# Kernel tuning notes

Hardware: AMD Instinct MI355X
Metric: run time of the kernel (lower is better)

Reference implementation:

```python
import jax, jax.numpy as jnp
import numpy as np

E = 32      # particle_embed_dim = q/k/v head out dim
G = 2       # nof_net_types (conv groups)
NEG_SLOPE = 0.01


def _glin(x, w, b, groups):
    """Grouped 1x1 conv on (M, C, 1, 1) == grouped linear.
    x: (M, Cin), w: (Cout, Cin//groups), b: (Cout,)."""
    M = x.shape[0]
    Cout = w.shape[0]
    xg = x.reshape(M, groups, -1)                 # (M, G, Cin/G)
    wg = w.reshape(groups, Cout // groups, -1)    # (G, Cout/G, Cin/G)
    y = jnp.einsum('mgi,goi->mgo', xg, wg).reshape(M, Cout)
    return y + b


def setup_inputs() -> dict:
    key = jax.random.key(0)
    ks = jax.random.split(key, 9)
    B, N = 32, 1024
    s = 0.05
    return {
        'x_e':   jax.random.normal(ks[0], (B, N, G * E), dtype=jnp.float32),
        'w_qkv': jax.random.normal(ks[1], (3 * G * E, E), dtype=jnp.float32) * s,
        'b_qkv': jax.random.normal(ks[2], (3 * G * E,), dtype=jnp.float32) * s,
        'w_h1':  jax.random.normal(ks[3], (G * E, 2 * E), dtype=jnp.float32) * s,
        'b_h1':  jax.random.normal(ks[4], (G * E,), dtype=jnp.float32) * s,
        'w_h10': jax.random.normal(ks[5], (G * E, E), dtype=jnp.float32) * s,
        'b_h10': jax.random.normal(ks[6], (G * E,), dtype=jnp.float32) * s,
        'w_h11': jax.random.normal(ks[7], (G * E, E), dtype=jnp.float32) * s,
        'b_h11': jax.random.normal(ks[8], (G * E,), dtype=jnp.float32) * s,
    }


def reference(x_e, w_qkv, b_qkv, w_h1, b_h1, w_h10, b_h10, w_h11, b_h11):
    B, N, D = x_e.shape                      # D = G*E = 64
    act = lambda z: jnp.where(z >= 0, z, NEG_SLOPE * z)

    # grouped 1x1-conv QKV projection
    qkv = _glin(x_e.reshape(B * N, D), w_qkv, b_qkv, G)        # (B*N, 3*G*E)
    qkv = qkv.reshape(B, N, G, 3, E).transpose(0, 2, 3, 1, 4)  # (B, G, 3, N, E)
    q, k, v = qkv[:, :, 0], qkv[:, :, 1], qkv[:, :, 2]         # each (B, G, N, E)

    # NOTE: module divides k by sqrt(E) and logits by sqrt(E) again -> 1/E total
    scale = 1.0 / E
    ip = jnp.einsum('bgne,bgme->bgnm', q, k) * scale           # (B, G, N, N)
    sip = jax.nn.softmax(ip, axis=-1)
    attn = jnp.einsum('bgnm,bgme->bgne', sip, v)               # (B, G, N, E)

    # concat pre-attention v with attention output, regroup per-particle
    x_xe = jnp.concatenate([v, attn], axis=3)                  # (B, G, N, 2E)
    x_xe = x_xe.transpose(0, 2, 1, 3).reshape(B * N, G * 2 * E)  # (B*N, 128)

    h = act(_glin(x_xe, w_h1, b_h1, G))
    h = act(_glin(h, w_h10, b_h10, G))
    h = act(_glin(h, w_h11, b_h11, G))
    return h.reshape(B * N, G * E, 1, 1)
```

## Files before the change

### kernel.cpp

```cpp
#include <hip/hip_runtime.h>

#define B_ 32
#define N_ 1024
#define G_ 2
#define E_ 32
#define M_ (B_*N_)
#define NEG 0.01f
#define QT 128
#define KT 128
#define QSC (1.4426950408889634f/32.0f)

using half8  = __attribute__((ext_vector_type(8))) _Float16;
using half4  = __attribute__((ext_vector_type(4))) _Float16;
using floatx4 = __attribute__((ext_vector_type(4))) float;

#if defined(__has_builtin)
#if __has_builtin(__builtin_amdgcn_exp2f)
#define EXP2(x) __builtin_amdgcn_exp2f(x)
#endif
#endif
#ifndef EXP2
#define EXP2(x) exp2f(x)
#endif

__global__ __launch_bounds__(256) void qkv_kernel(
    const float* __restrict__ x, const float* __restrict__ w, const float* __restrict__ bias,
    _Float16* __restrict__ Qh, _Float16* __restrict__ Kh,
    _Float16* __restrict__ Vh, _Float16* __restrict__ Vth)
{
    __shared__ _Float16 wsh[192*36];
    __shared__ float bsh[192];
    int t = threadIdx.x;
    for (int idx = t; idx < 192*32; idx += 256) {
        int r = idx >> 5, c = idx & 31;
        wsh[r*36 + c] = (_Float16)w[idx];
    }
    if (t < 192) bsh[t] = bias[t];
    __syncthreads();

    int lane = t & 63, wv = t >> 6;
    int L15 = lane & 15, quad = lane >> 4;
    int row0 = blockIdx.x*64 + wv*16;
    int b = row0 >> 10, nn0 = row0 & 1023;

    half4 ax[2][2];
    #pragma unroll
    for (int g2 = 0; g2 < 2; g2++)
        #pragma unroll
        for (int kt = 0; kt < 2; kt++) {
            float4 f = *(const float4*)(x + (size_t)(row0+L15)*64 + g2*32 + kt*16 + quad*4);
            half4 h = { (_Float16)f.x, (_Float16)f.y, (_Float16)f.z, (_Float16)f.w };
            ax[g2][kt] = h;
        }

    floatx4 acc[12];
    #pragma unroll
    for (int i = 0; i < 12; i++) acc[i] = (floatx4){0.f,0.f,0.f,0.f};

    #pragma unroll
    for (int g2 = 0; g2 < 2; g2++)
        #pragma unroll
        for (int nt = 0; nt < 6; nt++)
            #pragma unroll
            for (int kt = 0; kt < 2; kt++) {
                half4 bw = *(const half4*)&wsh[(g2*96+nt*16+L15)*36 + kt*16 + quad*4];
                acc[g2*6+nt] = __builtin_amdgcn_mfma_f32_16x16x16f16(ax[g2][kt], bw, acc[g2*6+nt], 0,0,0);
            }

    #pragma unroll
    for (int g2 = 0; g2 < 2; g2++) {
        size_t bg = (size_t)(b*2 + g2);
        #pragma unroll
        for (int nt = 0; nt < 6; nt++) {
            float bia = bsh[g2*96 + nt*16 + L15];
            floatx4 a4 = acc[g2*6+nt];
            int e = (nt & 1)*16 + L15;
            int kind = nt >> 1;
            if (kind == 0) {
                #pragma unroll
                for (int r = 0; r < 4; r++) {
                    int nn = nn0 + quad*4 + r;
                    Qh[(bg*N_ + nn)*32 + e] = (_Float16)((a4[r] + bia)*QSC);
                }
            } else if (kind == 1) {
                #pragma unroll
                for (int r = 0; r < 4; r++) {
                    int nn = nn0 + quad*4 + r;
                    Kh[(bg*N_ + nn)*32 + e] = (_Float16)(a4[r] + bia);
                }
            } else {
                half4 vv;
                #pragma unroll
                for (int r = 0; r < 4; r++) {
                    int nn = nn0 + quad*4 + r;
                    float vval = a4[r] + bia;
                    Vh[(bg*N_ + nn)*32 + e] = (_Float16)vval;
                    vv[r] = (_Float16)vval;
                }
                *(half4*)(Vth + (bg*32 + e)*N_ + nn0 + quad*4) = vv;
            }
        }
    }
}

struct __align__(16) SmemU {
    union {
        struct { _Float16 Kst[128*40]; _Float16 Vtst[32*136]; } a;
        _Float16 xs[128*72];
    } u;
    float linv[128];
    float bl1[32], bl10[32], bl11[32];
};

__global__ __launch_bounds__(256) void attn_mlp_kernel(
    const _Float16* __restrict__ Qh, const _Float16* __restrict__ Kh,
    const _Float16* __restrict__ Vh, const _Float16* __restrict__ Vth,
    const float* __restrict__ w_h1,  const float* __restrict__ b_h1,
    const float* __restrict__ w_h10, const float* __restrict__ b_h10,
    const float* __restrict__ w_h11, const float* __restrict__ b_h11,
    float* __restrict__ out)
{
    __shared__ SmemU sm;
    int t = threadIdx.x;
    int bg = blockIdx.x >> 3;
    int qtile = blockIdx.x & 7;
    int b = bg >> 1, g = bg & 1;
    int qbase = qtile * QT;
    size_t bgN = (size_t)bg * N_;

    if (t < 32) {
        sm.bl1[t]  = b_h1[g*32+t];
        sm.bl10[t] = b_h10[g*32+t];
        sm.bl11[t] = b_h11[g*32+t];
    }

    int lane = t & 63;
    int w    = t >> 6;
    int L15  = lane & 15;
    int quad = lane >> 4;
    int q0w  = qbase + w*32;

    half8 bq0 = *(const half8*)(Qh + (bgN + q0w +      L15)*32 + quad*8);
    half8 bq1 = *(const half8*)(Qh + (bgN + q0w + 16 + L15)*32 + quad*8);

    floatx4 o00 = {0.f,0.f,0.f,0.f}, o01 = o00, o10 = o00, o11 = o00;
    float lsum0 = 0.f, lsum1 = 0.f;

    for (int kt = 0; kt < N_/KT; kt++) {
        __syncthreads();
        #pragma unroll
        for (int it = 0; it < 2; it++) {
            int idx = t + it*256;
            int row = idx >> 2, c = idx & 3;
            half8 kv = *(const half8*)(Kh + (bgN + (size_t)kt*KT + row)*32 + c*8);
            *(half8*)&sm.u.a.Kst[row*40 + c*8] = kv;
        }
        #pragma unroll
        for (int it = 0; it < 2; it++) {
            int idx = t + it*256;
            int ee = idx >> 4, c = idx & 15;
            half8 vv = *(const half8*)(Vth + (size_t)bg*(32*N_) + (size_t)ee*N_ + kt*KT + c*8);
            *(half8*)&sm.u.a.Vtst[ee*136 + c*8] = vv;
        }
        __syncthreads();

        #pragma unroll
        for (int mt = 0; mt < 8; mt++) {
            half8 ak = *(const half8*)&sm.u.a.Kst[(mt*16 + L15)*40 + quad*8];
            floatx4 z = {0.f,0.f,0.f,0.f};
            floatx4 s0 = __builtin_amdgcn_mfma_f32_16x16x32_f16(ak, bq0, z, 0, 0, 0);
            floatx4 s1 = __builtin_amdgcn_mfma_f32_16x16x32_f16(ak, bq1, z, 0, 0, 0);
            float p00 = EXP2(s0.x), p01 = EXP2(s0.y), p02 = EXP2(s0.z), p03 = EXP2(s0.w);
            float p10 = EXP2(s1.x), p11 = EXP2(s1.y), p12 = EXP2(s1.z), p13 = EXP2(s1.w);
            lsum0 += (p00+p01)+(p02+p03);
            lsum1 += (p10+p11)+(p12+p13);
            half4 a0 = { (_Float16)p00, (_Float16)p01, (_Float16)p02, (_Float16)p03 };
            half4 a1 = { (_Float16)p10, (_Float16)p11, (_Float16)p12, (_Float16)p13 };
            half4 bv0 = *(const half4*)&sm.u.a.Vtst[      L15*136 + mt*16 + quad*4];
            half4 bv1 = *(const half4*)&sm.u.a.Vtst[(16+L15)*136 + mt*16 + quad*4];
            o00 = __builtin_amdgcn_mfma_f32_16x16x16f16(a0, bv0, o00, 0, 0, 0);
            o01 = __builtin_amdgcn_mfma_f32_16x16x16f16(a0, bv1, o01, 0, 0, 0);
            o10 = __builtin_amdgcn_mfma_f32_16x16x16f16(a1, bv0, o10, 0, 0, 0);
            o11 = __builtin_amdgcn_mfma_f32_16x16x16f16(a1, bv1, o11, 0, 0, 0);
        }
    }

    lsum0 += __shfl_xor(lsum0, 16, 64); lsum0 += __shfl_xor(lsum0, 32, 64);
    lsum1 += __shfl_xor(lsum1, 16, 64); lsum1 += __shfl_xor(lsum1, 32, 64);
    if (quad == 0) {
        sm.linv[w*32 +      L15] = 1.0f / lsum0;
        sm.linv[w*32 + 16 + L15] = 1.0f / lsum1;
    }
    __syncthreads();

    for (int idx = t; idx < 512; idx += 256) {
        int row = idx >> 2, c = idx & 3;
        half8 vv = *(const half8*)(Vh + (bgN + qbase + row)*32 + c*8);
        *(half8*)&sm.u.xs[row*72 + c*8] = vv;
    }
    {
        const floatx4* ofr[2][2] = { {&o00,&o01}, {&o10,&o11} };
        #pragma unroll
        for (int nt = 0; nt < 2; nt++) {
            float4 li = *(const float4*)&sm.linv[w*32 + nt*16 + quad*4];
            #pragma unroll
            for (int et = 0; et < 2; et++) {
                floatx4 ov = *ofr[nt][et];
                sm.u.xs[(w*32+nt*16+quad*4+0)*72 + 32 + et*16 + L15] = (_Float16)(ov[0]*li.x);
                sm.u.xs[(w*32+nt*16+quad*4+1)*72 + 32 + et*16 + L15] = (_Float16)(ov[1]*li.y);
                sm.u.xs[(w*32+nt*16+quad*4+2)*72 + 32 + et*16 + L15] = (_Float16)(ov[2]*li.z);
                sm.u.xs[(w*32+nt*16+quad*4+3)*72 + 32 + et*16 + L15] = (_Float16)(ov[3]*li.w);
            }
        }
    }
    __syncthreads();

    half4 a1f[2][4], a2f[2][2], a3f[2][2];
    #pragma unroll
    for (int mt = 0; mt < 2; mt++) {
        #pragma unroll
        for (int kt = 0; kt < 4; kt++) {
            float4 f = *(const float4*)(w_h1 + (size_t)(g*32+mt*16+L15)*64 + kt*16 + quad*4);
            half4 h = { (_Float16)f.x, (_Float16)f.y, (_Float16)f.z, (_Float16)f.w };
            a1f[mt][kt] = h;
        }
        #pragma unroll
        for (int kt = 0; kt < 2; kt++) {
            float4 f = *(const float4*)(w_h10 + (size_t)(g*32+mt*16+L15)*32 + kt*16 + quad*4);
            half4 h = { (_Float16)f.x, (_Float16)f.y, (_Float16)f.z, (_Float16)f.w };
            a2f[mt][kt] = h;
            float4 f2 = *(const float4*)(w_h11 + (size_t)(g*32+mt*16+L15)*32 + kt*16 + quad*4);
            half4 h2 = { (_Float16)f2.x, (_Float16)f2.y, (_Float16)f2.z, (_Float16)f2.w };
            a3f[mt][kt] = h2;
        }
    }

    floatx4 d1[2][2];
    #pragma unroll
    for (int mt = 0; mt < 2; mt++)
        #pragma unroll
        for (int nt = 0; nt < 2; nt++) d1[mt][nt] = (floatx4){0.f,0.f,0.f,0.f};
    #pragma unroll
    for (int nt = 0; nt < 2; nt++)
        #pragma unroll
        for (int kt = 0; kt < 4; kt++) {
            half4 b1 = *(const half4*)&sm.u.xs[(w*32+nt*16+L15)*72 + kt*16 + quad*4];
            d1[0][nt] = __builtin_amdgcn_mfma_f32_16x16x16f16(a1f[0][kt], b1, d1[0][nt], 0,0,0);
            d1[1][nt] = __builtin_amdgcn_mfma_f32_16x16x16f16(a1f[1][kt], b1, d1[1][nt], 0,0,0);
        }
    half4 h1b[2][2];
    #pragma unroll
    for (int mt = 0; mt < 2; mt++) {
        float4 bb = *(const float4*)&sm.bl1[mt*16 + quad*4];
        #pragma unroll
        for (int nt = 0; nt < 2; nt++) {
            float v0 = d1[mt][nt][0] + bb.x; v0 = (v0>=0.f)?v0:NEG*v0;
            float v1 = d1[mt][nt][1] + bb.y; v1 = (v1>=0.f)?v1:NEG*v1;
            float v2 = d1[mt][nt][2] + bb.z; v2 = (v2>=0.f)?v2:NEG*v2;
            float v3 = d1[mt][nt][3] + bb.w; v3 = (v3>=0.f)?v3:NEG*v3;
            half4 h = { (_Float16)v0, (_Float16)v1, (_Float16)v2, (_Float16)v3 };
            h1b[mt][nt] = h;
        }
    }
    floatx4 d2[2][2];
    #pragma unroll
    for (int mt = 0; mt < 2; mt++)
        #pragma unroll
        for (int nt = 0; nt < 2; nt++) d2[mt][nt] = (floatx4){0.f,0.f,0.f,0.f};
    #pragma unroll
    for (int mt = 0; mt < 2; mt++)
        #pragma unroll
        for (int nt = 0; nt < 2; nt++)
            #pragma unroll
            for (int kt = 0; kt < 2; kt++)
                d2[mt][nt] = __builtin_amdgcn_mfma_f32_16x16x16f16(a2f[mt][kt], h1b[kt][nt], d2[mt][nt], 0,0,0);
    half4 h2b[2][2];
    #pragma unroll
    for (int mt = 0; mt < 2; mt++) {
        float4 bb = *(const float4*)&sm.bl10[mt*16 + quad*4];
        #pragma unroll
        for (int nt = 0; nt < 2; nt++) {
            float v0 = d2[mt][nt][0] + bb.x; v0 = (v0>=0.f)?v0:NEG*v0;
            float v1 = d2[mt][nt][1] + bb.y; v1 = (v1>=0.f)?v1:NEG*v1;
            float v2 = d2[mt][nt][2] + bb.z; v2 = (v2>=0.f)?v2:NEG*v2;
            float v3 = d2[mt][nt][3] + bb.w; v3 = (v3>=0.f)?v3:NEG*v3;
            half4 h = { (_Float16)v0, (_Float16)v1, (_Float16)v2, (_Float16)v3 };
            h2b[mt][nt] = h;
        }
    }
    floatx4 d3[2][2];
    #pragma unroll
    for (int mt = 0; mt < 2; mt++)
        #pragma unroll
        for (int nt = 0; nt < 2; nt++) d3[mt][nt] = (floatx4){0.f,0.f,0.f,0.f};
    #pragma unroll
    for (int mt = 0; mt < 2; mt++)
        #pragma unroll
        for (int nt = 0; nt < 2; nt++)
            #pragma unroll
            for (int kt = 0; kt < 2; kt++)
                d3[mt][nt] = __builtin_amdgcn_mfma_f32_16x16x16f16(a3f[mt][kt], h2b[kt][nt], d3[mt][nt], 0,0,0);
    #pragma unroll
    for (int mt = 0; mt < 2; mt++) {
        float4 bb = *(const float4*)&sm.bl11[mt*16 + quad*4];
        #pragma unroll
        for (int nt = 0; nt < 2; nt++) {
            size_t rowbase = ((size_t)b*N_ + qbase + w*32 + nt*16 + L15)*64 + g*32 + mt*16 + quad*4;
            float v0 = d3[mt][nt][0] + bb.x; out[rowbase+0] = (v0>=0.f)?v0:NEG*v0;
            float v1 = d3[mt][nt][1] + bb.y; out[rowbase+1] = (v1>=0.f)?v1:NEG*v1;
            float v2 = d3[mt][nt][2] + bb.z; out[rowbase+2] = (v2>=0.f)?v2:NEG*v2;
            float v3 = d3[mt][nt][3] + bb.w; out[rowbase+3] = (v3>=0.f)?v3:NEG*v3;
        }
    }
}

extern "C" void kernel_launch(void* const* d_in, const int* in_sizes, int n_in,
                              void* d_out, int out_size, void* d_ws, size_t ws_size,
                              hipStream_t stream) {
    const float* x_e   = (const float*)d_in[0];
    const float* w_qkv = (const float*)d_in[1];
    const float* b_qkv = (const float*)d_in[2];
    const float* w_h1  = (const float*)d_in[3];
    const float* b_h1  = (const float*)d_in[4];
    const float* w_h10 = (const float*)d_in[5];
    const float* b_h10 = (const float*)d_in[6];
    const float* w_h11 = (const float*)d_in[7];
    const float* b_h11 = (const float*)d_in[8];
    float* out = (float*)d_out;

    const size_t qkv_elems = (size_t)B_*G_*N_*E_;
    _Float16* Qh  = (_Float16*)d_ws;
    _Float16* Kh  = Qh + qkv_elems;
    _Float16* Vh  = Kh + qkv_elems;
    _Float16* Vth = Vh + qkv_elems;

    hipLaunchKernelGGL(qkv_kernel, dim3(M_/64), dim3(256), 0, stream,
                       x_e, w_qkv, b_qkv, Qh, Kh, Vh, Vth);
    hipLaunchKernelGGL(attn_mlp_kernel, dim3(B_*G_*(N_/QT)), dim3(256), 0, stream,
                       Qh, Kh, Vh, Vth, w_h1, b_h1, w_h10, b_h10, w_h11, b_h11, out);
}
```

Measured before the change: 105.7 us.

## Double-buffer K/V tiles, stage QKV stores through LDS, pack conversions

The attention loop now double-buffers the K and V-transpose tiles in shared memory, loading the next tile into registers while the current one is computed, which removes one barrier per iteration. The QKV kernel stages Q/K/V/Vt in LDS and writes them with coalesced 16-byte stores instead of scattered 2-byte stores. Packed fp32->fp16 round-toward-zero conversions replace scalar casts, MLP biases seed the accumulators, and output stores become float4. Shared memory use grows, and launch_bounds now requests two blocks per CU, which may limit registers; rtz rounding slightly changes numerics.

```diff
diff --git a/kernel.cpp b/kernel.cpp
--- a/kernel.cpp
+++ b/kernel.cpp
@@ -2,16 +2,13 @@
 
 #define B_ 32
 #define N_ 1024
-#define G_ 2
-#define E_ 32
-#define M_ (B_*N_)
 #define NEG 0.01f
-#define QT 128
-#define KT 128
 #define QSC (1.4426950408889634f/32.0f)
 
 using half8  = __attribute__((ext_vector_type(8))) _Float16;
 using half4  = __attribute__((ext_vector_type(4))) _Float16;
+using half2  = __attribute__((ext_vector_type(2))) _Float16;
+using fp16x2 = __attribute__((ext_vector_type(2))) __fp16;
 using floatx4 = __attribute__((ext_vector_type(4))) float;
 
 #if defined(__has_builtin)
@@ -23,6 +20,11 @@
 #define EXP2(x) exp2f(x)
 #endif
 
+__device__ inline half2 pkcvt(float a, float b) {
+    fp16x2 r = __builtin_amdgcn_cvt_pkrtz(a, b);
+    return __builtin_bit_cast(half2, r);
+}
+
 __global__ __launch_bounds__(256) void qkv_kernel(
     const float* __restrict__ x, const float* __restrict__ w, const float* __restrict__ bias,
     _Float16* __restrict__ Qh, _Float16* __restrict__ Kh,
@@ -30,6 +32,8 @@
 {
     __shared__ _Float16 wsh[192*36];
     __shared__ float bsh[192];
+    __shared__ _Float16 sQ[64*72], sK[64*72], sV[64*72];
+    __shared__ _Float16 vT[64*72];
     int t = threadIdx.x;
     for (int idx = t; idx < 192*32; idx += 256) {
         int r = idx >> 5, c = idx & 31;
@@ -41,7 +45,7 @@
     int lane = t & 63, wv = t >> 6;
     int L15 = lane & 15, quad = lane >> 4;
     int row0 = blockIdx.x*64 + wv*16;
-    int b = row0 >> 10, nn0 = row0 & 1023;
+    int b = row0 >> 10, nn0g = (blockIdx.x*64) & 1023;
 
     half4 ax[2][2];
     #pragma unroll
@@ -49,7 +53,9 @@
         #pragma unroll
         for (int kt = 0; kt < 2; kt++) {
             float4 f = *(const float4*)(x + (size_t)(row0+L15)*64 + g2*32 + kt*16 + quad*4);
-            half4 h = { (_Float16)f.x, (_Float16)f.y, (_Float16)f.z, (_Float16)f.w };
+            half2 ha = pkcvt(f.x, f.y);
+            half2 hb = pkcvt(f.z, f.w);
+            half4 h = { ha[0], ha[1], hb[0], hb[1] };
             ax[g2][kt] = h;
         }
 
@@ -69,50 +75,60 @@
 
     #pragma unroll
     for (int g2 = 0; g2 < 2; g2++) {
-        size_t bg = (size_t)(b*2 + g2);
         #pragma unroll
         for (int nt = 0; nt < 6; nt++) {
             float bia = bsh[g2*96 + nt*16 + L15];
             floatx4 a4 = acc[g2*6+nt];
             int e = (nt & 1)*16 + L15;
             int kind = nt >> 1;
+            int rbase = wv*16 + quad*4;
             if (kind == 0) {
                 #pragma unroll
-                for (int r = 0; r < 4; r++) {
-                    int nn = nn0 + quad*4 + r;
-                    Qh[(bg*N_ + nn)*32 + e] = (_Float16)((a4[r] + bia)*QSC);
-                }
+                for (int r = 0; r < 4; r++)
+                    sQ[(rbase+r)*72 + g2*32 + e] = (_Float16)((a4[r] + bia)*QSC);
             } else if (kind == 1) {
                 #pragma unroll
-                for (int r = 0; r < 4; r++) {
-                    int nn = nn0 + quad*4 + r;
-                    Kh[(bg*N_ + nn)*32 + e] = (_Float16)(a4[r] + bia);
-                }
+                for (int r = 0; r < 4; r++)
+                    sK[(rbase+r)*72 + g2*32 + e] = (_Float16)(a4[r] + bia);
             } else {
                 half4 vv;
                 #pragma unroll
                 for (int r = 0; r < 4; r++) {
-                    int nn = nn0 + quad*4 + r;
                     float vval = a4[r] + bia;
-                    Vh[(bg*N_ + nn)*32 + e] = (_Float16)vval;
+                    sV[(rbase+r)*72 + g2*32 + e] = (_Float16)vval;
                     vv[r] = (_Float16)vval;
                 }
-                *(half4*)(Vth + (bg*32 + e)*N_ + nn0 + quad*4) = vv;
+                *(half4*)&vT[(g2*32+e)*72 + rbase] = vv;
             }
         }
     }
+    __syncthreads();
+
+    int r = t >> 2, c8 = t & 3;
+    #pragma unroll
+    for (int g2 = 0; g2 < 2; g2++) {
+        size_t gbase = (((size_t)(b*2+g2))*N_ + nn0g + r)*32 + c8*8;
+        *(half8*)(Qh + gbase) = *(const half8*)&sQ[r*72 + g2*32 + c8*8];
+        *(half8*)(Kh + gbase) = *(const half8*)&sK[r*72 + g2*32 + c8*8];
+        *(half8*)(Vh + gbase) = *(const half8*)&sV[r*72 + g2*32 + c8*8];
+    }
+    #pragma unroll
+    for (int it = 0; it < 2; it++) {
+        int idx = t + it*256;
+        int ge = idx >> 3, c = idx & 7;
+        *(half8*)(Vth + ((size_t)(b*2)*32 + ge)*N_ + nn0g + c*8) = *(const half8*)&vT[ge*72 + c*8];
+    }
 }
 
-struct __align__(16) SmemU {
-    union {
-        struct { _Float16 Kst[128*40]; _Float16 Vtst[32*136]; } a;
-        _Float16 xs[128*72];
-    } u;
+struct __align__(16) SmemB {
+    _Float16 Kst[2][128*40];
+    _Float16 Vtst[2][32*136];
+    _Float16 xs[128*72];
     float linv[128];
     float bl1[32], bl10[32], bl11[32];
 };
 
-__global__ __launch_bounds__(256) void attn_mlp_kernel(
+__global__ __launch_bounds__(256, 2) void attn_mlp_kernel(
     const _Float16* __restrict__ Qh, const _Float16* __restrict__ Kh,
     const _Float16* __restrict__ Vh, const _Float16* __restrict__ Vth,
     const float* __restrict__ w_h1,  const float* __restrict__ b_h1,
@@ -120,13 +136,15 @@
     const float* __restrict__ w_h11, const float* __restrict__ b_h11,
     float* __restrict__ out)
 {
-    __shared__ SmemU sm;
+    __shared__ SmemB sm;
     int t = threadIdx.x;
     int bg = blockIdx.x >> 3;
     int qtile = blockIdx.x & 7;
     int b = bg >> 1, g = bg & 1;
-    int qbase = qtile * QT;
+    int qbase = qtile * 128;
     size_t bgN = (size_t)bg * N_;
+    int lane = t & 63, w = t >> 6;
+    int L15 = lane & 15, quad = lane >> 4;
 
     if (t < 32) {
         sm.bl1[t]  = b_h1[g*32+t];
@@ -134,55 +152,65 @@
         sm.bl11[t] = b_h11[g*32+t];
     }
 
-    int lane = t & 63;
-    int w    = t >> 6;
-    int L15  = lane & 15;
-    int quad = lane >> 4;
-    int q0w  = qbase + w*32;
-
-    half8 bq0 = *(const half8*)(Qh + (bgN + q0w +      L15)*32 + quad*8);
-    half8 bq1 = *(const half8*)(Qh + (bgN + q0w + 16 + L15)*32 + quad*8);
-
-    floatx4 o00 = {0.f,0.f,0.f,0.f}, o01 = o00, o10 = o00, o11 = o00;
-    float lsum0 = 0.f, lsum1 = 0.f;
-
-    for (int kt = 0; kt < N_/KT; kt++) {
-        __syncthreads();
+    half8 bq0 = *(const half8*)(Qh + (bgN + qbase + w*32 +      L15)*32 + quad*8);
+    half8 bq1 = *(const half8*)(Qh + (bgN + qbase + w*32 + 16 + L15)*32 + quad*8);
+
+    float4 kr[2], vr[2];
+    auto ld = [&](int kt) {
         #pragma unroll
         for (int it = 0; it < 2; it++) {
             int idx = t + it*256;
             int row = idx >> 2, c = idx & 3;
-            half8 kv = *(const half8*)(Kh + (bgN + (size_t)kt*KT + row)*32 + c*8);
-            *(half8*)&sm.u.a.Kst[row*40 + c*8] = kv;
-        }
+            kr[it] = *(const float4*)(Kh + (bgN + (size_t)kt*128 + row)*32 + c*8);
+            int e = idx >> 4, cc = idx & 15;
+            vr[it] = *(const float4*)(Vth + ((size_t)bg*32 + e)*N_ + (size_t)kt*128 + cc*8);
+        }
+    };
+    auto st = [&](int buf) {
         #pragma unroll
         for (int it = 0; it < 2; it++) {
             int idx = t + it*256;
-            int ee = idx >> 4, c = idx & 15;
-            half8 vv = *(const half8*)(Vth + (size_t)bg*(32*N_) + (size_t)ee*N_ + kt*KT + c*8);
-            *(half8*)&sm.u.a.Vtst[ee*136 + c*8] = vv;
-        }
-        __syncthreads();
-
-        #pragma unroll
-        for (int mt = 0; mt < 8; mt++) {
-            half8 ak = *(const half8*)&sm.u.a.Kst[(mt*16 + L15)*40 + quad*8];
-            floatx4 z = {0.f,0.f,0.f,0.f};
-            floatx4 s0 = __builtin_amdgcn_mfma_f32_16x16x32_f16(ak, bq0, z, 0, 0, 0);
-            floatx4 s1 = __builtin_amdgcn_mfma_f32_16x16x32_f16(ak, bq1, z, 0, 0, 0);
+            int row = idx >> 2, c = idx & 3;
+            *(float4*)&sm.Kst[buf][row*40 + c*8] = kr[it];
+            int e = idx >> 4, cc = idx & 15;
+            *(float4*)&sm.Vtst[buf][e*136 + cc*8] = vr[it];
+        }
+    };
+
+    ld(0); st(0);
+    __syncthreads();
+
+    floatx4 o00 = {0.f,0.f,0.f,0.f}, o01 = o00, o10 = o00, o11 = o00;
+    float lsum0 = 0.f, lsum1 = 0.f;
+
+    for (int kt = 0; kt < 8; kt++) {
+        int cur = kt & 1;
+        if (kt < 7) ld(kt + 1);
+        #pragma unroll
+        for (int m8 = 0; m8 < 8; m8++) {
+            half8 ak = *(const half8*)&sm.Kst[cur][(m8*16 + L15)*40 + quad*8];
+            floatx4 zz = {0.f,0.f,0.f,0.f};
+            floatx4 s0 = __builtin_amdgcn_mfma_f32_16x16x32_f16(ak, bq0, zz, 0,0,0);
+            floatx4 s1 = __builtin_amdgcn_mfma_f32_16x16x32_f16(ak, bq1, zz, 0,0,0);
             float p00 = EXP2(s0.x), p01 = EXP2(s0.y), p02 = EXP2(s0.z), p03 = EXP2(s0.w);
             float p10 = EXP2(s1.x), p11 = EXP2(s1.y), p12 = EXP2(s1.z), p13 = EXP2(s1.w);
             lsum0 += (p00+p01)+(p02+p03);
             lsum1 += (p10+p11)+(p12+p13);
-            half4 a0 = { (_Float16)p00, (_Float16)p01, (_Float16)p02, (_Float16)p03 };
-            half4 a1 = { (_Float16)p10, (_Float16)p11, (_Float16)p12, (_Float16)p13 };
-            half4 bv0 = *(const half4*)&sm.u.a.Vtst[      L15*136 + mt*16 + quad*4];
-            half4 bv1 = *(const half4*)&sm.u.a.Vtst[(16+L15)*136 + mt*16 + quad*4];
-            o00 = __builtin_amdgcn_mfma_f32_16x16x16f16(a0, bv0, o00, 0, 0, 0);
-            o01 = __builtin_amdgcn_mfma_f32_16x16x16f16(a0, bv1, o01, 0, 0, 0);
-            o10 = __builtin_amdgcn_mfma_f32_16x16x16f16(a1, bv0, o10, 0, 0, 0);
-            o11 = __builtin_amdgcn_mfma_f32_16x16x16f16(a1, bv1, o11, 0, 0, 0);
-        }
+            half2 pa = pkcvt(p00, p01);
+            half2 pb = pkcvt(p02, p03);
+            half2 pc = pkcvt(p10, p11);
+            half2 pd = pkcvt(p12, p13);
+            half4 a0 = { pa[0], pa[1], pb[0], pb[1] };
+            half4 a1 = { pc[0], pc[1], pd[0], pd[1] };
+            half4 bv0 = *(const half4*)&sm.Vtst[cur][      L15*136 + m8*16 + quad*4];
+            half4 bv1 = *(const half4*)&sm.Vtst[cur][(16 + L15)*136 + m8*16 + quad*4];
+            o00 = __builtin_amdgcn_mfma_f32_16x16x16f16(a0, bv0, o00, 0,0,0);
+            o01 = __builtin_amdgcn_mfma_f32_16x16x16f16(a0, bv1, o01, 0,0,0);
+            o10 = __builtin_amdgcn_mfma_f32_16x16x16f16(a1, bv0, o10, 0,0,0);
+            o11 = __builtin_amdgcn_mfma_f32_16x16x16f16(a1, bv1, o11, 0,0,0);
+        }
+        if (kt < 7) st(1 - cur);
+        __syncthreads();
     }
 
     lsum0 += __shfl_xor(lsum0, 16, 64); lsum0 += __shfl_xor(lsum0, 32, 64);
@@ -191,12 +219,12 @@
         sm.linv[w*32 +      L15] = 1.0f / lsum0;
         sm.linv[w*32 + 16 + L15] = 1.0f / lsum1;
     }
-    __syncthreads();
-
-    for (int idx = t; idx < 512; idx += 256) {
+
+    #pragma unroll
+    for (int it = 0; it < 2; it++) {
+        int idx = t + it*256;
         int row = idx >> 2, c = idx & 3;
-        half8 vv = *(const half8*)(Vh + (bgN + qbase + row)*32 + c*8);
-        *(half8*)&sm.u.xs[row*72 + c*8] = vv;
+        *(half8*)&sm.xs[row*72 + c*8] = *(const half8*)(Vh + (bgN + qbase + row)*32 + c*8);
     }
     {
         const floatx4* ofr[2][2] = { {&o00,&o01}, {&o10,&o11} };
@@ -206,10 +234,10 @@
             #pragma unroll
             for (int et = 0; et < 2; et++) {
                 floatx4 ov = *ofr[nt][et];
-                sm.u.xs[(w*32+nt*16+quad*4+0)*72 + 32 + et*16 + L15] = (_Float16)(ov[0]*li.x);
-                sm.u.xs[(w*32+nt*16+quad*4+1)*72 + 32 + et*16 + L15] = (_Float16)(ov[1]*li.y);
-                sm.u.xs[(w*32+nt*16+quad*4+2)*72 + 32 + et*16 + L15] = (_Float16)(ov[2]*li.z);
-                sm.u.xs[(w*32+nt*16+quad*4+3)*72 + 32 + et*16 + L15] = (_Float16)(ov[3]*li.w);
+                sm.xs[(w*32+nt*16+quad*4+0)*72 + 32 + et*16 + L15] = (_Float16)(ov[0]*li.x);
+                sm.xs[(w*32+nt*16+quad*4+1)*72 + 32 + et*16 + L15] = (_Float16)(ov[1]*li.y);
+                sm.xs[(w*32+nt*16+quad*4+2)*72 + 32 + et*16 + L15] = (_Float16)(ov[2]*li.z);
+                sm.xs[(w*32+nt*16+quad*4+3)*72 + 32 + et*16 + L15] = (_Float16)(ov[3]*li.w);
             }
         }
     }
@@ -221,52 +249,62 @@
         #pragma unroll
         for (int kt = 0; kt < 4; kt++) {
             float4 f = *(const float4*)(w_h1 + (size_t)(g*32+mt*16+L15)*64 + kt*16 + quad*4);
-            half4 h = { (_Float16)f.x, (_Float16)f.y, (_Float16)f.z, (_Float16)f.w };
+            half2 ha = pkcvt(f.x, f.y);
+            half2 hb = pkcvt(f.z, f.w);
+            half4 h = { ha[0], ha[1], hb[0], hb[1] };
             a1f[mt][kt] = h;
         }
         #pragma unroll
         for (int kt = 0; kt < 2; kt++) {
             float4 f = *(const float4*)(w_h10 + (size_t)(g*32+mt*16+L15)*32 + kt*16 + quad*4);
-            half4 h = { (_Float16)f.x, (_Float16)f.y, (_Float16)f.z, (_Float16)f.w };
+            half2 ha = pkcvt(f.x, f.y);
+            half2 hb = pkcvt(f.z, f.w);
+            half4 h = { ha[0], ha[1], hb[0], hb[1] };
             a2f[mt][kt] = h;
             float4 f2 = *(const float4*)(w_h11 + (size_t)(g*32+mt*16+L15)*32 + kt*16 + quad*4);
-            half4 h2 = { (_Float16)f2.x, (_Float16)f2.y, (_Float16)f2.z, (_Float16)f2.w };
+            half2 hc = pkcvt(f2.x, f2.y);
+            half2 hd = pkcvt(f2.z, f2.w);
+            half4 h2 = { hc[0], hc[1], hd[0], hd[1] };
             a3f[mt][kt] = h2;
         }
     }
 
     floatx4 d1[2][2];
     #pragma unroll
-    for (int mt = 0; mt < 2; mt++)
-        #pragma unroll
-        for (int nt = 0; nt < 2; nt++) d1[mt][nt] = (floatx4){0.f,0.f,0.f,0.f};
+    for (int mt = 0; mt < 2; mt++) {
+        float4 bb = *(const float4*)&sm.bl1[mt*16 + quad*4];
+        floatx4 seed = { bb.x, bb.y, bb.z, bb.w };
+        d1[mt][0] = seed; d1[mt][1] = seed;
+    }
     #pragma unroll
     for (int nt = 0; nt < 2; nt++)
         #pragma unroll
         for (int kt = 0; kt < 4; kt++) {
-            half4 b1 = *(const half4*)&sm.u.xs[(w*32+nt*16+L15)*72 + kt*16 + quad*4];
+            half4 b1 = *(const half4*)&sm.xs[(w*32+nt*16+L15)*72 + kt*16 + quad*4];
             d1[0][nt] = __builtin_amdgcn_mfma_f32_16x16x16f16(a1f[0][kt], b1, d1[0][nt], 0,0,0);
             d1[1][nt] = __builtin_amdgcn_mfma_f32_16x16x16f16(a1f[1][kt], b1, d1[1][nt], 0,0,0);
         }
     half4 h1b[2][2];
     #pragma unroll
+    for (int mt = 0; mt < 2; mt++)
+        #pragma unroll
+        for (int nt = 0; nt < 2; nt++) {
+            float v0 = d1[mt][nt][0]; v0 = (v0>=0.f)?v0:NEG*v0;
+            float v1 = d1[mt][nt][1]; v1 = (v1>=0.f)?v1:NEG*v1;
+            float v2 = d1[mt][nt][2]; v2 = (v2>=0.f)?v2:NEG*v2;
+            float v3 = d1[mt][nt][3]; v3 = (v3>=0.f)?v3:NEG*v3;
+            half2 ha = pkcvt(v0, v1);
+            half2 hb = pkcvt(v2, v3);
+            half4 h = { ha[0], ha[1], hb[0], hb[1] };
+            h1b[mt][nt] = h;
+        }
+    floatx4 d2[2][2];
+    #pragma unroll
     for (int mt = 0; mt < 2; mt++) {
-        float4 bb = *(const float4*)&sm.bl1[mt*16 + quad*4];
-        #pragma unroll
-        for (int nt = 0; nt < 2; nt++) {
-            float v0 = d1[mt][nt][0] + bb.x; v0 = (v0>=0.f)?v0:NEG*v0;
-            float v1 = d1[mt][nt][1] + bb.y; v1 = (v1>=0.f)?v1:NEG*v1;
-            float v2 = d1[mt][nt][2] + bb.z; v2 = (v2>=0.f)?v2:NEG*v2;
-            float v3 = d1[mt][nt][3] + bb.w; v3 = (v3>=0.f)?v3:NEG*v3;
-            half4 h = { (_Float16)v0, (_Float16)v1, (_Float16)v2, (_Float16)v3 };
-            h1b[mt][nt] = h;
-        }
-    }
-    floatx4 d2[2][2];
-    #pragma unroll
-    for (int mt = 0; mt < 2; mt++)
-        #pragma unroll
-        for (int nt = 0; nt < 2; nt++) d2[mt][nt] = (floatx4){0.f,0.f,0.f,0.f};
+        float4 bb = *(const float4*)&sm.bl10[mt*16 + quad*4];
+        floatx4 seed = { bb.x, bb.y, bb.z, bb.w };
+        d2[mt][0] = seed; d2[mt][1] = seed;
+    }
     #pragma unroll
     for (int mt = 0; mt < 2; mt++)
         #pragma unroll
@@ -276,23 +314,25 @@
                 d2[mt][nt] = __builtin_amdgcn_mfma_f32_16x16x16f16(a2f[mt][kt], h1b[kt][nt], d2[mt][nt], 0,0,0);
     half4 h2b[2][2];
     #pragma unroll
+    for (int mt = 0; mt < 2; mt++)
+        #pragma unroll
+        for (int nt = 0; nt < 2; nt++) {
+            float v0 = d2[mt][nt][0]; v0 = (v0>=0.f)?v0:NEG*v0;
+            float v1 = d2[mt][nt][1]; v1 = (v1>=0.f)?v1:NEG*v1;
+            float v2 = d2[mt][nt][2]; v2 = (v2>=0.f)?v2:NEG*v2;
+            float v3 = d2[mt][nt][3]; v3 = (v3>=0.f)?v3:NEG*v3;
+            half2 ha = pkcvt(v0, v1);
+            half2 hb = pkcvt(v2, v3);
+            half4 h = { ha[0], ha[1], hb[0], hb[1] };
+            h2b[mt][nt] = h;
+        }
+    floatx4 d3[2][2];
+    #pragma unroll
     for (int mt = 0; mt < 2; mt++) {
-        float4 bb = *(const float4*)&sm.bl10[mt*16 + quad*4];
-        #pragma unroll
-        for (int nt = 0; nt < 2; nt++) {
-            float v0 = d2[mt][nt][0] + bb.x; v0 = (v0>=0.f)?v0:NEG*v0;
-            float v1 = d2[mt][nt][1] + bb.y; v1 = (v1>=0.f)?v1:NEG*v1;
-            float v2 = d2[mt][nt][2] + bb.z; v2 = (v2>=0.f)?v2:NEG*v2;
-            float v3 = d2[mt][nt][3] + bb.w; v3 = (v3>=0.f)?v3:NEG*v3;
-            half4 h = { (_Float16)v0, (_Float16)v1, (_Float16)v2, (_Float16)v3 };
-            h2b[mt][nt] = h;
-        }
-    }
-    floatx4 d3[2][2];
-    #pragma unroll
-    for (int mt = 0; mt < 2; mt++)
-        #pragma unroll
-        for (int nt = 0; nt < 2; nt++) d3[mt][nt] = (floatx4){0.f,0.f,0.f,0.f};
+        float4 bb = *(const float4*)&sm.bl11[mt*16 + quad*4];
+        floatx4 seed = { bb.x, bb.y, bb.z, bb.w };
+        d3[mt][0] = seed; d3[mt][1] = seed;
+    }
     #pragma unroll
     for (int mt = 0; mt < 2; mt++)
         #pragma unroll
@@ -301,17 +341,16 @@
             for (int kt = 0; kt < 2; kt++)
                 d3[mt][nt] = __builtin_amdgcn_mfma_f32_16x16x16f16(a3f[mt][kt], h2b[kt][nt], d3[mt][nt], 0,0,0);
     #pragma unroll
-    for (int mt = 0; mt < 2; mt++) {
-        float4 bb = *(const float4*)&sm.bl11[mt*16 + quad*4];
+    for (int mt = 0; mt < 2; mt++)
         #pragma unroll
         for (int nt = 0; nt < 2; nt++) {
-            size_t rowbase = ((size_t)b*N_ + qbase + w*32 + nt*16 + L15)*64 + g*32 + mt*16 + quad*4;
-            float v0 = d3[mt][nt][0] + bb.x; out[rowbase+0] = (v0>=0.f)?v0:NEG*v0;
-            float v1 = d3[mt][nt][1] + bb.y; out[rowbase+1] = (v1>=0.f)?v1:NEG*v1;
-            float v2 = d3[mt][nt][2] + bb.z; out[rowbase+2] = (v2>=0.f)?v2:NEG*v2;
-            float v3 = d3[mt][nt][3] + bb.w; out[rowbase+3] = (v3>=0.f)?v3:NEG*v3;
-        }
-    }
+            float4 ov;
+            ov.x = d3[mt][nt][0]; ov.x = (ov.x>=0.f)?ov.x:NEG*ov.x;
+            ov.y = d3[mt][nt][1]; ov.y = (ov.y>=0.f)?ov.y:NEG*ov.y;
+            ov.z = d3[mt][nt][2]; ov.z = (ov.z>=0.f)?ov.z:NEG*ov.z;
+            ov.w = d3[mt][nt][3]; ov.w = (ov.w>=0.f)?ov.w:NEG*ov.w;
+            *(float4*)(out + ((size_t)b*N_ + qbase + w*32 + nt*16 + L15)*64 + g*32 + mt*16 + quad*4) = ov;
+        }
 }
 
 extern "C" void kernel_launch(void* const* d_in, const int* in_sizes, int n_in,
@@ -328,14 +367,14 @@
     const float* b_h11 = (const float*)d_in[8];
     float* out = (float*)d_out;
 
-    const size_t qkv_elems = (size_t)B_*G_*N_*E_;
+    const size_t qkv_elems = (size_t)B_*2*N_*32;
     _Float16* Qh  = (_Float16*)d_ws;
     _Float16* Kh  = Qh + qkv_elems;
     _Float16* Vh  = Kh + qkv_elems;
     _Float16* Vth = Vh + qkv_elems;
 
-    hipLaunchKernelGGL(qkv_kernel, dim3(M_/64), dim3(256), 0, stream,
+    hipLaunchKernelGGL(qkv_kernel, dim3((B_*N_)/64), dim3(256), 0, stream,
                        x_e, w_qkv, b_qkv, Qh, Kh, Vh, Vth);
-    hipLaunchKernelGGL(attn_mlp_kernel, dim3(B_*G_*(N_/QT)), dim3(256), 0, stream,
+    hipLaunchKernelGGL(attn_mlp_kernel, dim3(B_*2*8), dim3(256), 0, stream,
                        Qh, Kh, Vh, Vth, w_h1, b_h1, w_h10, b_h10, w_h11, b_h11, out);
 }
```

After: 124.3 us. +17.6%, slower.
